# Kernel optimization log

Hardware: AMD Instinct MI355X
Metric: run time of the kernel (lower is better)

The kernel has to match this reference:

```python
import jax, jax.numpy as jnp
import numpy as np

S = 3072      # total packed tokens
D = 1536      # hidden_size
H = 12        # num_heads
HD = D // H   # head_dim = 128
NSEQ = 4      # number of packed sequences (images)


def rotate_half(x):
    x1 = x[..., : x.shape[-1] // 2]
    x2 = x[..., x.shape[-1] // 2 :]
    return jnp.concatenate((-x2, x1), axis=-1)


def setup_inputs() -> dict:
    key = jax.random.key(0)
    k1, k2, k3 = jax.random.split(key, 3)
    hidden_states = jax.random.normal(k1, (S, D), jnp.float32)
    # 4 equal-length packed sequences
    cu_seqlens = (jnp.arange(NSEQ + 1, dtype=jnp.int32) * (S // NSEQ))
    # RoPE cos/sin per token, period within each packed sequence
    pos = (jnp.arange(S) % (S // NSEQ)).astype(jnp.float32)
    inv_freq = 1.0 / (10000.0 ** (jnp.arange(0, HD // 2, dtype=jnp.float32) / (HD // 2)))
    freqs = pos[:, None] * inv_freq[None, :]          # [S, HD//2]
    emb = jnp.concatenate([freqs, freqs], axis=-1)    # [S, HD]
    cos, sin = jnp.cos(emb), jnp.sin(emb)
    qkv_w = jax.random.normal(k2, (3 * D, D), jnp.float32) * (D ** -0.5)
    qkv_b = jnp.zeros((3 * D,), jnp.float32)
    proj_w = jax.random.normal(k3, (D, D), jnp.float32) * (D ** -0.5)
    return {
        "hidden_states": hidden_states,
        "cos": cos,
        "sin": sin,
        "qkv_w": qkv_w,
        "qkv_b": qkv_b,
        "proj_w": proj_w,
        "cu_seqlens": cu_seqlens,
    }


def reference(hidden_states, cos, sin, qkv_w, qkv_b, proj_w, cu_seqlens):
    s_len, dim = hidden_states.shape
    # fused QKV projection -> [S, 3, H, HD]
    qkv = (hidden_states @ qkv_w.T + qkv_b).reshape(s_len, 3, H, HD)
    q, k, v = qkv[:, 0], qkv[:, 1], qkv[:, 2]         # each [S, H, HD]
    # inline RoPE (fp32, broadcast over heads)
    c = cos[:, None, :].astype(jnp.float32)
    s = sin[:, None, :].astype(jnp.float32)
    qf, kf = q.astype(jnp.float32), k.astype(jnp.float32)
    q = (qf * c + rotate_half(qf) * s).astype(q.dtype)
    k = (kf * c + rotate_half(kf) * s).astype(k.dtype)
    # block-diagonal (varlen) mask from cu_seqlens
    seg = jnp.searchsorted(cu_seqlens, jnp.arange(s_len), side="right")  # [S]
    same_seq = seg[:, None] == seg[None, :]                              # [S, S]
    bias = jnp.where(same_seq, 0.0, -jnp.inf).astype(jnp.float32)
    scaling = HD ** -0.5
    # scores [H, S, S]
    scores = jnp.einsum("shd,thd->hst", q, k) * scaling + bias[None]
    probs = jax.nn.softmax(scores.astype(jnp.float32), axis=-1).astype(q.dtype)
    attn = jnp.einsum("hst,thd->shd", probs, v).reshape(s_len, dim)
    return attn @ proj_w.T
```

## Files before the change

### kernel.cpp

```cpp
#include <hip/hip_runtime.h>
#include <stdint.h>

#define S_LEN 3072
#define DIM   1536
#define NH    12
#define HD    128
#define QKV_N 4608

typedef unsigned short u16;
typedef __bf16 bf16x8 __attribute__((ext_vector_type(8)));
typedef float  f32x4  __attribute__((ext_vector_type(4)));
typedef u16    u16x8  __attribute__((ext_vector_type(8)));

#define AS1 __attribute__((address_space(1)))
#define AS3 __attribute__((address_space(3)))
#define GLL16(g, l) __builtin_amdgcn_global_load_lds((AS1 void*)(g), (AS3 void*)(l), 16, 0, 0)

__device__ __forceinline__ u16 f2bf(float f) {
  unsigned u = __float_as_uint(f);
  u = (u + 0x7fffu + ((u >> 16) & 1u)) >> 16;
  return (u16)u;
}
__device__ __forceinline__ float bf2f(u16 b) {
  return __uint_as_float(((unsigned)b) << 16);
}

__global__ __launch_bounds__(256) void cvt_bf16(const float* __restrict__ in,
                                                u16* __restrict__ out, int n4) {
  int stride = gridDim.x * blockDim.x;
  for (int i = blockIdx.x * blockDim.x + threadIdx.x; i < n4; i += stride) {
    float4 v = ((const float4*)in)[i];
    ushort4 o;
    o.x = f2bf(v.x); o.y = f2bf(v.y); o.z = f2bf(v.z); o.w = f2bf(v.w);
    ((ushort4*)out)[i] = o;
  }
}

__device__ __forceinline__ bf16x8 lds_frag(const u16* base, int row, int ch) {
  return *(const bf16x8*)(base + row * 64 + ((ch ^ row) & 7) * 8);
}

__global__ __launch_bounds__(512) void gemm_bt_256(const u16* __restrict__ A,
                                                   const u16* __restrict__ B,
                                                   const float* __restrict__ bias,
                                                   u16* __restrict__ Cout,
                                                   int M, int N, int K) {
  __shared__ __attribute__((aligned(16))) u16 lds[2 * 2 * 256 * 64];

  const int t = threadIdx.x;
  const int l = t & 63;
  const int w = t >> 6;
  const int wm = w >> 2;
  const int wn = w & 3;

  const int nbx = N >> 8;
  const int nwg = gridDim.x;
  const int q = nwg >> 3, r = nwg & 7;
  const int xcd = blockIdx.x & 7, rest = blockIdx.x >> 3;
  const int wgid = (xcd < r ? xcd * (q + 1) : r * (q + 1) + (xcd - r) * q) + rest;
  const int m0 = (wgid / nbx) * 256;
  const int n0 = (wgid % nbx) * 256;

  const int nk = K >> 6;

  f32x4 acc[8][4];
  #pragma unroll
  for (int i = 0; i < 8; ++i)
    #pragma unroll
    for (int j = 0; j < 4; ++j) acc[i][j] = f32x4{0.f, 0.f, 0.f, 0.f};

  auto stage = [&](int c, int kt) {
    #pragma unroll
    for (int i = 0; i < 8; ++i) {
      int C = t + i * 512;
      int ab = C >> 11;
      int CC = C & 2047;
      int row = CC >> 3, ch = CC & 7;
      int sch = (ch ^ row) & 7;
      const u16* src = (ab ? B + (size_t)(n0 + row) * K
                           : A + (size_t)(m0 + row) * K) + kt * 64 + sch * 8;
      GLL16(src, lds + c * 32768 + ab * 16384 + CC * 8);
    }
  };

  int c = 0;
  stage(0, 0);
  __syncthreads();

  for (int kt = 0; kt < nk; ++kt) {
    if (kt + 1 < nk) stage(c ^ 1, kt + 1);

    const u16* Ab = lds + c * 32768;
    const u16* Bb = Ab + 16384;

    bf16x8 bfrag[4][2];
    #pragma unroll
    for (int ni = 0; ni < 4; ++ni)
      #pragma unroll
      for (int ks = 0; ks < 2; ++ks)
        bfrag[ni][ks] = lds_frag(Bb, wn * 64 + ni * 16 + (l & 15), ks * 4 + (l >> 4));

    #pragma unroll
    for (int p = 0; p < 4; ++p) {
      bf16x8 af[2][2];
      #pragma unroll
      for (int mi = 0; mi < 2; ++mi)
        #pragma unroll
        for (int ks = 0; ks < 2; ++ks)
          af[mi][ks] = lds_frag(Ab, wm * 128 + (p * 2 + mi) * 16 + (l & 15),
                                ks * 4 + (l >> 4));
      __builtin_amdgcn_s_setprio(1);
      #pragma unroll
      for (int ks = 0; ks < 2; ++ks)
        #pragma unroll
        for (int mi = 0; mi < 2; ++mi)
          #pragma unroll
          for (int ni = 0; ni < 4; ++ni)
            acc[p * 2 + mi][ni] = __builtin_amdgcn_mfma_f32_16x16x32_bf16(
                af[mi][ks], bfrag[ni][ks], acc[p * 2 + mi][ni], 0, 0, 0);
      __builtin_amdgcn_s_setprio(0);
    }

    __syncthreads();
    c ^= 1;
  }

  #pragma unroll
  for (int ni = 0; ni < 4; ++ni) {
    int col = n0 + wn * 64 + ni * 16 + (l & 15);
    float bv = bias ? bias[col] : 0.f;
    #pragma unroll
    for (int mi = 0; mi < 8; ++mi) {
      int rbase = m0 + wm * 128 + mi * 16 + ((l >> 4) << 2);
      #pragma unroll
      for (int rr = 0; rr < 4; ++rr)
        Cout[(size_t)(rbase + rr) * N + col] = f2bf(acc[mi][ni][rr] + bv);
    }
  }
}

template <bool BIAS, bool OUTF32>
__global__ __launch_bounds__(256) void gemm_bt(const u16* __restrict__ A,
                                               const u16* __restrict__ B,
                                               const float* __restrict__ bias,
                                               void* __restrict__ Cout,
                                               int M, int N, int K) {
  __shared__ u16 Asm[128 * 64];
  __shared__ u16 Bsm[128 * 64];
  const int t = threadIdx.x;
  const int l = t & 63;
  const int w = t >> 6;
  const int wm = w >> 1, wn = w & 1;
  const int m0 = blockIdx.y * 128, n0 = blockIdx.x * 128;

  f32x4 acc[4][4];
  #pragma unroll
  for (int i = 0; i < 4; ++i)
    #pragma unroll
    for (int j = 0; j < 4; ++j) acc[i][j] = f32x4{0.f, 0.f, 0.f, 0.f};

  for (int k0 = 0; k0 < K; k0 += 64) {
    __syncthreads();
    #pragma unroll
    for (int r4 = 0; r4 < 4; ++r4) {
      int C = t + r4 * 256;
      int row = C >> 3, ch = C & 7;
      int sch = (ch ^ row) & 7;
      GLL16(A + (size_t)(m0 + row) * K + k0 + sch * 8, Asm + (size_t)C * 8);
      GLL16(B + (size_t)(n0 + row) * K + k0 + sch * 8, Bsm + (size_t)C * 8);
    }
    __syncthreads();
    #pragma unroll
    for (int ks = 0; ks < 2; ++ks) {
      bf16x8 af[4], bfr[4];
      #pragma unroll
      for (int mi = 0; mi < 4; ++mi)
        af[mi] = lds_frag(Asm, wm * 64 + mi * 16 + (l & 15), ks * 4 + (l >> 4));
      #pragma unroll
      for (int ni = 0; ni < 4; ++ni)
        bfr[ni] = lds_frag(Bsm, wn * 64 + ni * 16 + (l & 15), ks * 4 + (l >> 4));
      #pragma unroll
      for (int mi = 0; mi < 4; ++mi)
        #pragma unroll
        for (int ni = 0; ni < 4; ++ni)
          acc[mi][ni] = __builtin_amdgcn_mfma_f32_16x16x32_bf16(af[mi], bfr[ni],
                                                                acc[mi][ni], 0, 0, 0);
    }
  }

  #pragma unroll
  for (int ni = 0; ni < 4; ++ni) {
    int col = n0 + wn * 64 + ni * 16 + (l & 15);
    float bv = 0.f;
    if (BIAS) bv = bias[col];
    #pragma unroll
    for (int mi = 0; mi < 4; ++mi) {
      int rbase = m0 + wm * 64 + mi * 16 + ((l >> 4) << 2);
      #pragma unroll
      for (int rr = 0; rr < 4; ++rr) {
        float v = acc[mi][ni][rr] + bv;
        if (OUTF32)
          ((float*)Cout)[(size_t)(rbase + rr) * N + col] = v;
        else
          ((u16*)Cout)[(size_t)(rbase + rr) * N + col] = f2bf(v);
      }
    }
  }
}

__global__ __launch_bounds__(256) void rope_pack(const u16* __restrict__ QKV,
                                                 const float* __restrict__ cosb,
                                                 const float* __restrict__ sinb,
                                                 u16* __restrict__ Qp,
                                                 u16* __restrict__ Kp,
                                                 u16* __restrict__ Vt) {
  __shared__ u16 vtile[64][128];
  const int t = threadIdx.x;
  const int s0 = blockIdx.x * 64;
  const int h = blockIdx.y;

  const int srow = s0 + (t >> 2);
  const int d0 = (t & 3) * 16;
  const u16* qkvrow = QKV + (size_t)srow * QKV_N + h * HD;
  const float qscale = 0.08838834764831845f * 1.4426950408889634f;
  #pragma unroll
  for (int which = 0; which < 2; ++which) {
    const u16* src = qkvrow + which * DIM;
    u16* dst = (which ? Kp : Qp) + ((size_t)h * S_LEN + srow) * HD;
    const float sc = which ? 1.f : qscale;
    #pragma unroll
    for (int j = 0; j < 16; ++j) {
      int d = d0 + j;
      float xlo = bf2f(src[d]);
      float xhi = bf2f(src[d + 64]);
      float clo = cosb[srow * HD + d], chi = cosb[srow * HD + d + 64];
      float slo = sinb[srow * HD + d], shi = sinb[srow * HD + d + 64];
      dst[d]      = f2bf((xlo * clo - xhi * slo) * sc);
      dst[d + 64] = f2bf((xhi * chi + xlo * shi) * sc);
    }
  }

  #pragma unroll
  for (int r4 = 0; r4 < 4; ++r4) {
    int C = t + r4 * 256;
    int row = C >> 4, ch = C & 15;
    *(uint4*)(&vtile[row][ch * 8]) =
        *(const uint4*)(QKV + (size_t)(s0 + row) * QKV_N + 2 * DIM + h * HD + ch * 8);
  }
  __syncthreads();
  const int d = t >> 1;
  const int sc0 = (t & 1) * 32;
  u16* vdst = Vt + ((size_t)h * HD + d) * S_LEN + s0 + sc0;
  #pragma unroll
  for (int j = 0; j < 32; j += 8) {
    u16x8 v;
    #pragma unroll
    for (int e = 0; e < 8; ++e) v[e] = vtile[sc0 + j + e][d];
    *(u16x8*)(vdst + j) = v;
  }
}

__global__ __launch_bounds__(256) void attn_fwd(const u16* __restrict__ Qp,
                                                const u16* __restrict__ Kp,
                                                const u16* __restrict__ Vt,
                                                const int* __restrict__ cu,
                                                u16* __restrict__ Obf) {
  __shared__ u16 K_lds[64 * 128];
  __shared__ u16 VT_lds[128 * 64];
  __shared__ u16 P_lds[4][16 * 72];

  const int t = threadIdx.x;
  const int l = t & 63;
  const int w = t >> 6;
  const int q0 = blockIdx.x * 64;
  const int h = blockIdx.y;

  int cs = 0, ce = S_LEN;
  #pragma unroll
  for (int b = 0; b < 4; ++b) {
    int lo = cu[b], hi = cu[b + 1];
    if (q0 >= lo && q0 < hi) { cs = lo; ce = hi; }
  }

  const int qrow = q0 + w * 16 + (l & 15);
  bf16x8 qf[4];
  const u16* qptr = Qp + ((size_t)h * S_LEN + qrow) * HD + ((l >> 4) * 8);
  #pragma unroll
  for (int ks = 0; ks < 4; ++ks) qf[ks] = *(const bf16x8*)(qptr + ks * 32);

  f32x4 acc_o[8];
  #pragma unroll
  for (int i = 0; i < 8; ++i) acc_o[i] = f32x4{0.f, 0.f, 0.f, 0.f};
  float m_run[4], l_run[4];
  #pragma unroll
  for (int r = 0; r < 4; ++r) { m_run[r] = -1e30f; l_run[r] = 0.f; }

  for (int kv0 = cs; kv0 < ce; kv0 += 64) {
    __syncthreads();
    {
      const u16* kbase = Kp + ((size_t)h * S_LEN + kv0) * HD;
      #pragma unroll
      for (int r4 = 0; r4 < 4; ++r4) {
        int C = t + r4 * 256;
        int row = C >> 4, ch = C & 15;
        int sch = (ch & 8) | ((ch ^ row) & 7);
        GLL16(kbase + row * HD + sch * 8, K_lds + (size_t)C * 8);
      }
      const u16* vbase = Vt + (size_t)h * HD * S_LEN + kv0;
      #pragma unroll
      for (int r4 = 0; r4 < 4; ++r4) {
        int C = t + r4 * 256;
        int row = C >> 3, ch = C & 7;
        int sch = (ch ^ row) & 7;
        GLL16(vbase + (size_t)row * S_LEN + sch * 8, VT_lds + (size_t)C * 8);
      }
    }
    __syncthreads();

    f32x4 s_acc[4];
    #pragma unroll
    for (int nf = 0; nf < 4; ++nf) {
      s_acc[nf] = f32x4{0.f, 0.f, 0.f, 0.f};
      int kcol = nf * 16 + (l & 15);
      #pragma unroll
      for (int ks = 0; ks < 4; ++ks) {
        int ch = ks * 4 + (l >> 4);
        int sch = (ch & 8) | ((ch ^ kcol) & 7);
        bf16x8 kf = *(const bf16x8*)(K_lds + kcol * 128 + sch * 8);
        s_acc[nf] = __builtin_amdgcn_mfma_f32_16x16x32_bf16(qf[ks], kf, s_acc[nf], 0, 0, 0);
      }
    }

    float p[4][4], alpha[4];
    #pragma unroll
    for (int r = 0; r < 4; ++r) {
      float v = fmaxf(fmaxf(s_acc[0][r], s_acc[1][r]), fmaxf(s_acc[2][r], s_acc[3][r]));
      #pragma unroll
      for (int m = 1; m < 16; m <<= 1) v = fmaxf(v, __shfl_xor(v, m, 64));
      float mn = fmaxf(m_run[r], v);
      alpha[r] = __builtin_amdgcn_exp2f(m_run[r] - mn);
      m_run[r] = mn;
      float sum = 0.f;
      #pragma unroll
      for (int nf = 0; nf < 4; ++nf) {
        float pv = __builtin_amdgcn_exp2f(s_acc[nf][r] - mn);
        p[nf][r] = pv;
        sum += pv;
      }
      #pragma unroll
      for (int m = 1; m < 16; m <<= 1) sum += __shfl_xor(sum, m, 64);
      l_run[r] = l_run[r] * alpha[r] + sum;
    }
    #pragma unroll
    for (int onf = 0; onf < 8; ++onf)
      #pragma unroll
      for (int r = 0; r < 4; ++r) acc_o[onf][r] *= alpha[r];

    u16* pl = P_lds[w];
    #pragma unroll
    for (int nf = 0; nf < 4; ++nf)
      #pragma unroll
      for (int r = 0; r < 4; ++r)
        pl[((l >> 4) * 4 + r) * 72 + nf * 16 + (l & 15)] = f2bf(p[nf][r]);

    #pragma unroll
    for (int ks = 0; ks < 2; ++ks) {
      bf16x8 pa = *(const bf16x8*)(pl + (l & 15) * 72 + ks * 32 + (l >> 4) * 8);
      #pragma unroll
      for (int onf = 0; onf < 8; ++onf) {
        int d = onf * 16 + (l & 15);
        int ch = ks * 4 + (l >> 4);
        int sch = (ch ^ d) & 7;
        bf16x8 vf = *(const bf16x8*)(VT_lds + d * 64 + sch * 8);
        acc_o[onf] = __builtin_amdgcn_mfma_f32_16x16x32_bf16(pa, vf, acc_o[onf], 0, 0, 0);
      }
    }
  }

  #pragma unroll
  for (int r = 0; r < 4; ++r) {
    float inv = 1.f / l_run[r];
    int srow = q0 + w * 16 + ((l >> 4) << 2) + r;
    u16* orow = Obf + (size_t)srow * DIM + h * HD + (l & 15);
    #pragma unroll
    for (int onf = 0; onf < 8; ++onf) orow[onf * 16] = f2bf(acc_o[onf][r] * inv);
  }
}

extern "C" void kernel_launch(void* const* d_in, const int* in_sizes, int n_in,
                              void* d_out, int out_size, void* d_ws, size_t ws_size,
                              hipStream_t stream) {
  const float* hidden = (const float*)d_in[0];
  const float* cosb   = (const float*)d_in[1];
  const float* sinb   = (const float*)d_in[2];
  const float* qkv_w  = (const float*)d_in[3];
  const float* qkv_b  = (const float*)d_in[4];
  const float* proj_w = (const float*)d_in[5];
  const int*   cu     = (const int*)d_in[6];

  u16* Hbf   = (u16*)d_ws;
  u16* Wqkv  = Hbf   + (size_t)S_LEN * DIM;
  u16* Wproj = Wqkv  + (size_t)QKV_N * DIM;
  u16* QKVbf = Wproj + (size_t)DIM * DIM;
  u16* Kp    = QKVbf + (size_t)S_LEN * QKV_N;
  u16* Vt    = Kp    + (size_t)NH * S_LEN * HD;
  u16* Qp    = Wqkv;
  u16* Abf   = Hbf;

  cvt_bf16<<<2048, 256, 0, stream>>>(hidden, Hbf, S_LEN * DIM / 4);
  cvt_bf16<<<2048, 256, 0, stream>>>(qkv_w, Wqkv, QKV_N * DIM / 4);
  cvt_bf16<<<2048, 256, 0, stream>>>(proj_w, Wproj, DIM * DIM / 4);

  gemm_bt_256<<<(S_LEN / 256) * (QKV_N / 256), 512, 0, stream>>>(
      Hbf, Wqkv, qkv_b, QKVbf, S_LEN, QKV_N, DIM);

  rope_pack<<<dim3(S_LEN / 64, NH), 256, 0, stream>>>(QKVbf, cosb, sinb, Qp, Kp, Vt);

  attn_fwd<<<dim3(S_LEN / 64, NH), 256, 0, stream>>>(Qp, Kp, Vt, cu, Abf);

  gemm_bt<false, true><<<dim3(DIM / 128, S_LEN / 128), 256, 0, stream>>>(
      Abf, Wproj, nullptr, d_out, S_LEN, DIM, DIM);
}
```

Measured before the change: 171.1 us.

## Split 256x256 GEMM k-tile into half-stages with fine-grained barrier pipelining

Restructures the 256x256 QKV GEMM main loop so each 64-wide k-tile is split into two 32-wide halves, each stored in its own LDS region with a new pair-row swizzle. Global-to-LDS loads for the next tile are issued in quarter pieces between MFMA phases, gated by explicit vmcnt waits and raw s_barrier instead of a full __syncthreads per tile. The goal is to overlap global loads with MFMA work and cut the register footprint so two workgroups fit per CU (launch_bounds 512,2). The cost is more barriers per iteration and a higher chance of ordering or occupancy issues.

```diff
diff --git a/kernel.cpp b/kernel.cpp
--- a/kernel.cpp
+++ b/kernel.cpp
@@ -36,22 +36,27 @@
   }
 }
 
-__device__ __forceinline__ bf16x8 lds_frag(const u16* base, int row, int ch) {
-  return *(const bf16x8*)(base + row * 64 + ((ch ^ row) & 7) * 8);
-}
-
-__global__ __launch_bounds__(512) void gemm_bt_256(const u16* __restrict__ A,
-                                                   const u16* __restrict__ B,
-                                                   const float* __restrict__ bias,
-                                                   u16* __restrict__ Cout,
-                                                   int M, int N, int K) {
-  __shared__ __attribute__((aligned(16))) u16 lds[2 * 2 * 256 * 64];
+
+__device__ __forceinline__ bf16x8 frag2(const u16* region, int row, int ch) {
+  int L = row >> 1;
+  int slot = ((ch + ((row & 1) << 2)) ^ L) & 7;
+  return *(const bf16x8*)(region + L * 64 + slot * 8);
+}
+
+__global__ __launch_bounds__(512, 2) void gemm_bt_256(const u16* __restrict__ A,
+                                                      const u16* __restrict__ B,
+                                                      const float* __restrict__ bias,
+                                                      u16* __restrict__ Cout,
+                                                      int M, int N, int K) {
+  __shared__ __attribute__((aligned(16))) u16 lds[8 * 8192];
 
   const int t = threadIdx.x;
   const int l = t & 63;
   const int w = t >> 6;
   const int wm = w >> 2;
   const int wn = w & 3;
+  const int lr = l & 15;
+  const int lc = l >> 4;
 
   const int nbx = N >> 8;
   const int nwg = gridDim.x;
@@ -69,74 +74,90 @@
     #pragma unroll
     for (int j = 0; j < 4; ++j) acc[i][j] = f32x4{0.f, 0.f, 0.f, 0.f};
 
-  auto stage = [&](int c, int kt) {
-    #pragma unroll
-    for (int i = 0; i < 8; ++i) {
+  auto stage_half = [&](int buf, int ks, int ab, int kt) {
+    const u16* base = ab ? B : A;
+    const int x0 = ab ? n0 : m0;
+    u16* dst = lds + (((buf << 2) | (ks << 1) | ab) * 8192);
+    #pragma unroll
+    for (int i = 0; i < 2; ++i) {
       int C = t + i * 512;
-      int ab = C >> 11;
-      int CC = C & 2047;
-      int row = CC >> 3, ch = CC & 7;
-      int sch = (ch ^ row) & 7;
-      const u16* src = (ab ? B + (size_t)(n0 + row) * K
-                           : A + (size_t)(m0 + row) * K) + kt * 64 + sch * 8;
-      GLL16(src, lds + c * 32768 + ab * 16384 + CC * 8);
+      int L = C >> 3, s = C & 7;
+      int u = s ^ (L & 7);
+      int row = 2 * L + (u >> 2), ch = u & 3;
+      const u16* src = base + (size_t)(x0 + row) * K + kt * 64 + ks * 32 + ch * 8;
+      GLL16(src, dst + C * 8);
     }
   };
 
-  int c = 0;
-  stage(0, 0);
-  __syncthreads();
+  stage_half(0, 0, 0, 0); stage_half(0, 0, 1, 0);
+  stage_half(0, 1, 0, 0); stage_half(0, 1, 1, 0);
+  asm volatile("s_waitcnt vmcnt(4)" ::: "memory");
+  __builtin_amdgcn_s_barrier();
 
   for (int kt = 0; kt < nk; ++kt) {
-    if (kt + 1 < nk) stage(c ^ 1, kt + 1);
-
-    const u16* Ab = lds + c * 32768;
-    const u16* Bb = Ab + 16384;
-
-    bf16x8 bfrag[4][2];
-    #pragma unroll
-    for (int ni = 0; ni < 4; ++ni)
-      #pragma unroll
-      for (int ks = 0; ks < 2; ++ks)
-        bfrag[ni][ks] = lds_frag(Bb, wn * 64 + ni * 16 + (l & 15), ks * 4 + (l >> 4));
-
-    #pragma unroll
-    for (int p = 0; p < 4; ++p) {
-      bf16x8 af[2][2];
-      #pragma unroll
-      for (int mi = 0; mi < 2; ++mi)
+    const int buf = kt & 1, nbuf = buf ^ 1;
+    const bool st = (kt + 1 < nk);
+
+    #pragma unroll
+    for (int ks = 0; ks < 2; ++ks) {
+      const u16* Ar = lds + (((buf << 2) | (ks << 1) | 0) * 8192);
+      const u16* Br = lds + (((buf << 2) | (ks << 1) | 1) * 8192);
+
+      bf16x8 bfrag[4], afr[4];
+      #pragma unroll
+      for (int ni = 0; ni < 4; ++ni) bfrag[ni] = frag2(Br, wn * 64 + ni * 16 + lr, lc);
+      #pragma unroll
+      for (int mi = 0; mi < 4; ++mi) afr[mi] = frag2(Ar, wm * 128 + mi * 16 + lr, lc);
+      if (st) stage_half(nbuf, ks, 0, kt + 1);
+      __builtin_amdgcn_s_barrier();
+      __builtin_amdgcn_s_setprio(1);
+      #pragma unroll
+      for (int mi = 0; mi < 4; ++mi)
         #pragma unroll
-        for (int ks = 0; ks < 2; ++ks)
-          af[mi][ks] = lds_frag(Ab, wm * 128 + (p * 2 + mi) * 16 + (l & 15),
-                                ks * 4 + (l >> 4));
+        for (int ni = 0; ni < 4; ++ni)
+          acc[mi][ni] = __builtin_amdgcn_mfma_f32_16x16x32_bf16(afr[mi], bfrag[ni],
+                                                                acc[mi][ni], 0, 0, 0);
+      __builtin_amdgcn_s_setprio(0);
+      __builtin_amdgcn_s_barrier();
+
+      #pragma unroll
+      for (int mi = 0; mi < 4; ++mi)
+        afr[mi] = frag2(Ar, wm * 128 + 64 + mi * 16 + lr, lc);
+      if (st) {
+        stage_half(nbuf, ks, 1, kt + 1);
+        asm volatile("s_waitcnt vmcnt(4)" ::: "memory");
+      } else {
+        asm volatile("s_waitcnt vmcnt(0)" ::: "memory");
+      }
+      __builtin_amdgcn_s_barrier();
       __builtin_amdgcn_s_setprio(1);
       #pragma unroll
-      for (int ks = 0; ks < 2; ++ks)
+      for (int mi = 0; mi < 4; ++mi)
         #pragma unroll
-        for (int mi = 0; mi < 2; ++mi)
-          #pragma unroll
-          for (int ni = 0; ni < 4; ++ni)
-            acc[p * 2 + mi][ni] = __builtin_amdgcn_mfma_f32_16x16x32_bf16(
-                af[mi][ks], bfrag[ni][ks], acc[p * 2 + mi][ni], 0, 0, 0);
+        for (int ni = 0; ni < 4; ++ni)
+          acc[4 + mi][ni] = __builtin_amdgcn_mfma_f32_16x16x32_bf16(afr[mi], bfrag[ni],
+                                                                    acc[4 + mi][ni], 0, 0, 0);
       __builtin_amdgcn_s_setprio(0);
-    }
-
-    __syncthreads();
-    c ^= 1;
+      __builtin_amdgcn_s_barrier();
+    }
   }
 
   #pragma unroll
   for (int ni = 0; ni < 4; ++ni) {
-    int col = n0 + wn * 64 + ni * 16 + (l & 15);
+    int col = n0 + wn * 64 + ni * 16 + lr;
     float bv = bias ? bias[col] : 0.f;
     #pragma unroll
     for (int mi = 0; mi < 8; ++mi) {
-      int rbase = m0 + wm * 128 + mi * 16 + ((l >> 4) << 2);
+      int rbase = m0 + wm * 128 + mi * 16 + (lc << 2);
       #pragma unroll
       for (int rr = 0; rr < 4; ++rr)
         Cout[(size_t)(rbase + rr) * N + col] = f2bf(acc[mi][ni][rr] + bv);
     }
   }
+}
+
+__device__ __forceinline__ bf16x8 lds_frag(const u16* base, int row, int ch) {
+  return *(const bf16x8*)(base + row * 64 + ((ch ^ row) & 7) * 8);
 }
 
 template <bool BIAS, bool OUTF32>
```

Result: no change. 172.6 us (+0.8%).
